# Kernel optimization log

Hardware: AMD Instinct MI355X
Metric: run time of the kernel (lower is better)

## Reference

```python
import jax, jax.numpy as jnp
import numpy as np

N, D, A, NQ, G1, G2 = 2048, 512, 64, 8, 8, 8
A1 = 2 * A  # tier-1 MQA uses att_dim*2 internally


def setup_inputs() -> dict:
    key = jax.random.key(0)
    ks = iter(jax.random.split(key, 24))
    r = lambda *sh: (jax.random.normal(next(ks), sh, dtype=jnp.float32) * 0.02)
    return {
        "x": jax.random.normal(next(ks), (N, D), dtype=jnp.float32),
        # tier 1 (num_groups_first MQA blocks, inner dim A1)
        "Wq1": r(G1, NQ, D, A1), "bq1": r(G1, NQ, A1),
        "Wk1": r(G1, D, A1),     "bk1": r(G1, A1),
        "Wv1": r(G1, D, A1),     "bv1": r(G1, A1),
        "Wo1": r(G1, NQ * A1, D), "bo1": r(G1, D),
        # tier 2 (num_groups_second MQA blocks, inner dim A)
        "Wq2": r(G2, NQ, D, A), "bq2": r(G2, NQ, A),
        "Wk2": r(G2, D, A),     "bk2": r(G2, A),
        "Wv2": r(G2, D, A),     "bv2": r(G2, A),
        "Wo2": r(G2, NQ * A, D), "bo2": r(G2, D),
        # final projection: in = att_dim * num_groups_second == D
        "Wo": r(D, D), "bo": r(D),
    }


def _mqa_grouped(xg, Wq, bq, Wk, bk, Wv, bv, Wo, bo):
    """Batched MultiQueryAttention over a group axis g.
    xg: [g, n, d]; Wq: [g, q, d, a]. No softmax (per source)."""
    a = Wq.shape[-1]
    q = jnp.einsum('gnd,gqda->gqna', xg, Wq) + bq[:, :, None, :]
    k = jnp.einsum('gnd,gda->gna', xg, Wk) + bk[:, None, :]
    v = jnp.einsum('gnd,gda->gna', xg, Wv) + bv[:, None, :]
    scores = jnp.einsum('gqna,gma->gqnm', q, k) / jnp.sqrt(jnp.asarray(a, jnp.float32))
    ctx = jnp.einsum('gqnm,gma->gqna', scores, v)          # [g,q,n,a]
    g, nq, n, ad = ctx.shape
    ctx = ctx.transpose(0, 2, 1, 3).reshape(g, n, nq * ad)  # concat queries on feat dim
    return jnp.einsum('gnf,gfd->gnd', ctx, Wo) + bo[:, None, :]


def reference(x, Wq1, bq1, Wk1, bk1, Wv1, bv1, Wo1, bo1,
              Wq2, bq2, Wk2, bk2, Wv2, bv2, Wo2, bo2, Wo, bo):
    xg = jnp.broadcast_to(x[None], (G1, N, D))
    o1 = _mqa_grouped(xg, Wq1, bq1, Wk1, bk1, Wv1, bv1, Wo1, bo1)   # [G1,N,D]
    o2 = _mqa_grouped(o1[:G2], Wq2, bq2, Wk2, bk2, Wv2, bv2, Wo2, bo2)  # [G2,N,D]
    o2_flat = o2.reshape(G2 * N, D)  # torch.cat along token dim (dim=0)
    return o2_flat @ Wo + bo          # [G2*N, D]
```

## Files before the change

kernel.cpp:

```cpp
#include <hip/hip_runtime.h>


typedef __bf16 bf16x8 __attribute__((ext_vector_type(8)));
typedef float  f32x4  __attribute__((ext_vector_type(4)));

struct PD { const float* s; void* d; int R, C, Bc, mode, blocks; };
struct PArgs { PD p[20]; int n; };

struct MA {
    const float *x,*bq1,*bo1,*bq2,*bo2,*bo;
    float* out;
    __bf16 *xb,*Wk1t,*Wv1t,*Wq1b,*Wo1t,*Wk2t,*Wv2t,*Wq2b,*Wo2b,*Wot;
    __bf16 *Ktb,*Vtb,*T1b,*M1t,*o1b,*K2tb,*V2tb,*T2b,*Wo2pT,*M2pt;
    float *STf1,*STf2,*kvb1,*kvb2,*c1,*c2p,*bo2p;
    PArgs pa;
    int prepTot;
};

template<int BM, int BN, int KK>
__device__ __forceinline__ void ss_gemm(void* smv,
    const __bf16* __restrict__ A, const float* __restrict__ Bf,
    __bf16* __restrict__ C, long aG, long bG, long cG, int cD, int cQ, int vb)
{
    constexpr int MT = BM / 32, NT = BN / 32, KS = KK / 32;
    constexpr int ACH = (KK * 2) / 16;
    constexpr int ABYTES = BM * KK * 2;
    constexpr int AITER = ABYTES / 16 / 256;
    constexpr int ROWB = KK * 2;
    constexpr int F4PT = (BN * KK) / 4 / 256;
    constexpr int TPR  = (KK / 4) / F4PT;

    char* smc = (char*)smv;
    int g = vb >> 6, rb = vb & 63;
    A  += g * aG + (long)rb * BM * KK;
    Bf += g * bG;
    C  += g * cG;

    int tid = threadIdx.x, wave = tid >> 6, lane = tid & 63;
    int mrow = lane & 15, quad = lane >> 4;

    #pragma unroll
    for (int i = 0; i < AITER; ++i) {
        int c = tid + i * 256;
        int row = c / ACH, cp = c % ACH;
        int cg = cp ^ (row & 7);
        __builtin_amdgcn_global_load_lds(
            (const __attribute__((address_space(1))) void*)(A + (long)row * KK + cg * 8),
            (__attribute__((address_space(3))) void*)(smc + c * 16),
            16, 0, 0);
    }
    {
        int brow = tid / TPR, bseg = tid % TPR;
        const float4* bsrc = (const float4*)(Bf + (long)brow * KK + bseg * (KK / TPR));
        int cbase = (bseg * (KK / TPR)) >> 3;
        int bx7 = brow & 7;
        char* bls = smc + ABYTES + (long)brow * ROWB;
        #pragma unroll
        for (int j = 0; j < F4PT / 2; ++j) {
            float4 f0 = bsrc[2 * j], f1 = bsrc[2 * j + 1];
            bf16x8 v = {(__bf16)f0.x, (__bf16)f0.y, (__bf16)f0.z, (__bf16)f0.w,
                        (__bf16)f1.x, (__bf16)f1.y, (__bf16)f1.z, (__bf16)f1.w};
            *(bf16x8*)(bls + (((cbase + j) ^ bx7) << 4)) = v;
        }
    }
    __syncthreads();

    int wm = (wave >> 1) * (BM / 2), wn = (wave & 1) * (BN / 2);
    f32x4 acc[MT][NT];
    #pragma unroll
    for (int i = 0; i < MT; ++i)
        #pragma unroll
        for (int j = 0; j < NT; ++j)
            acc[i][j] = f32x4{0.f, 0.f, 0.f, 0.f};

    #pragma unroll
    for (int ks = 0; ks < KS; ++ks) {
        bf16x8 af[MT], bv[NT];
        #pragma unroll
        for (int mt = 0; mt < MT; ++mt) {
            int r = wm + mt * 16 + mrow;
            af[mt] = *(const bf16x8*)(smc + (long)r * ROWB
                        + (((ks * 4 + quad) ^ (r & 7)) << 4));
        }
        #pragma unroll
        for (int nt = 0; nt < NT; ++nt) {
            int r = wn + nt * 16 + mrow;
            bv[nt] = *(const bf16x8*)(smc + ABYTES + (long)r * ROWB
                        + (((ks * 4 + quad) ^ (r & 7)) << 4));
        }
        #pragma unroll
        for (int mt = 0; mt < MT; ++mt)
            #pragma unroll
            for (int nt = 0; nt < NT; ++nt)
                acc[mt][nt] = __builtin_amdgcn_mfma_f32_16x16x32_bf16(
                    af[mt], bv[nt], acc[mt][nt], 0, 0, 0);
    }

    #pragma unroll
    for (int mt = 0; mt < MT; ++mt) {
        #pragma unroll
        for (int r4 = 0; r4 < 4; ++r4) {
            int rl = wm + mt * 16 + quad * 4 + r4;
            int ra = rb * BM + rl;
            int q = ra >> 9, d = ra & 511;
            #pragma unroll
            for (int nt = 0; nt < NT; ++nt) {
                int col = wn + nt * 16 + mrow;
                C[(long)d * cD + q * cQ + col] = (__bf16)acc[mt][nt][r4];
            }
        }
    }
}

template<int BM, int BN, bool BF32, int MODE>
__device__ __forceinline__ void gemm_block(void* smv,
    const __bf16* __restrict__ A, const void* __restrict__ Bv,
    const float* __restrict__ bias, void* __restrict__ Cv,
    int K, int lda, int ldb, int ldc, int divq, int ksplit,
    long aOut, long aIn, long bOut, long bIn, long cOut, long cIn,
    long biasOut, long biasIn, int hasBias, float alpha,
    int bx, int by, int bz)
{
    constexpr int MT = BM / 32, NT = BN / 32;
    constexpr int HALF = (BM + BN) * 64;
    constexpr int AL = BM / 64;
    constexpr int BL = BF32 ? 0 : BN / 64;

    char* smc = (char*)smv;

    int b  = bz / ksplit, ks = bz - b * ksplit;
    int go = b / divq,  gi = b - go * divq;
    A += go * aOut + gi * aIn;
    const __bf16* Bb = (const __bf16*)Bv + (BF32 ? 0 : (go * bOut + gi * bIn));
    const float*  Bf = (const float*)Bv + (BF32 ? (go * bOut + gi * bIn) : 0);
    long cBase = go * cOut + gi * cIn;
    if (hasBias) bias += go * biasOut + gi * biasIn;

    int kChunk = K / ksplit;
    int k0 = ks * kChunk;
    int nT = kChunk / 32;

    int bm = by * BM, bn = bx * BN;
    int tid = threadIdx.x, wave = tid >> 6, lane = tid & 63;
    int wm = (wave >> 1) * (BM / 2), wn = (wave & 1) * (BN / 2);
    int mrow = lane & 15, quad = lane >> 4;

    f32x4 acc[MT][NT];
    #pragma unroll
    for (int i = 0; i < MT; ++i)
        #pragma unroll
        for (int j = 0; j < NT; ++j)
            acc[i][j] = f32x4{0.f, 0.f, 0.f, 0.f};

    float4 bf0, bf1;
    int brow = tid >> 2, bcb = (tid & 3) * 8;

    auto loadBf32 = [&](int kk) {
        const float* src = Bf + (long)(bn + brow) * ldb + kk + bcb;
        bf0 = *(const float4*)(src);
        bf1 = *(const float4*)(src + 4);
    };
    auto writeBf32 = [&](int buf) {
        bf16x8 v = {(__bf16)bf0.x, (__bf16)bf0.y, (__bf16)bf0.z, (__bf16)bf0.w,
                    (__bf16)bf1.x, (__bf16)bf1.y, (__bf16)bf1.z, (__bf16)bf1.w};
        *(bf16x8*)(smc + buf * HALF + BM * 64 + brow * 64 + bcb * 2) = v;
    };
    auto issueAB = [&](int buf, int kk) {
        char* base = smc + buf * HALF;
        #pragma unroll
        for (int t = 0; t < AL; ++t) {
            int c = tid + t * 256;
            int row = c >> 2, kq = c & 3;
            __builtin_amdgcn_global_load_lds(
                (const __attribute__((address_space(1))) void*)
                    (A + (long)(bm + row) * lda + kk + kq * 8),
                (__attribute__((address_space(3))) void*)(base + row * 64 + kq * 16),
                16, 0, 0);
        }
        if constexpr (!BF32) {
            #pragma unroll
            for (int t = 0; t < BL; ++t) {
                int c = tid + t * 256;
                int row = c >> 2, kq = c & 3;
                __builtin_amdgcn_global_load_lds(
                    (const __attribute__((address_space(1))) void*)
                        (Bb + (long)(bn + row) * ldb + kk + kq * 8),
                    (__attribute__((address_space(3))) void*)
                        (base + BM * 64 + row * 64 + kq * 16),
                    16, 0, 0);
            }
        }
    };

    if constexpr (BF32) loadBf32(k0);
    issueAB(0, k0);
    if constexpr (BF32) writeBf32(0);
    __syncthreads();

    int cur = 0;
    for (int t = 0; t < nT; ++t) {
        int kk = k0 + (t + 1) * 32;
        if (t + 1 < nT) {
            if constexpr (BF32) loadBf32(kk);
            issueAB(cur ^ 1, kk);
        }

        char* base = smc + cur * HALF;
        bf16x8 af[MT], bfv[NT];
        #pragma unroll
        for (int mt = 0; mt < MT; ++mt)
            af[mt] = *(const bf16x8*)(base + (wm + mt * 16 + mrow) * 64 + quad * 16);
        #pragma unroll
        for (int nt = 0; nt < NT; ++nt)
            bfv[nt] = *(const bf16x8*)(base + BM * 64 + (wn + nt * 16 + mrow) * 64 + quad * 16);
        #pragma unroll
        for (int mt = 0; mt < MT; ++mt)
            #pragma unroll
            for (int nt = 0; nt < NT; ++nt) {
                if constexpr (MODE == 2)
                    acc[mt][nt] = __builtin_amdgcn_mfma_f32_16x16x32_bf16(
                        bfv[nt], af[mt], acc[mt][nt], 0, 0, 0);
                else
                    acc[mt][nt] = __builtin_amdgcn_mfma_f32_16x16x32_bf16(
                        af[mt], bfv[nt], acc[mt][nt], 0, 0, 0);
            }

        if constexpr (BF32) {
            if (t + 1 < nT) writeBf32(cur ^ 1);
        }

        __syncthreads();
        cur ^= 1;
    }

    if constexpr (MODE == 2) {
        #pragma unroll
        for (int nt = 0; nt < NT; ++nt) {
            #pragma unroll
            for (int r = 0; r < 4; ++r) {
                int ci = bn + wn + nt * 16 + quad * 4 + r;
                #pragma unroll
                for (int mt = 0; mt < MT; ++mt) {
                    int mi = bm + wm + mt * 16 + mrow;
                    float v = acc[mt][nt][r] * alpha;
                    if (hasBias) v += bias[ci];
                    ((__bf16*)Cv)[cBase + (long)ci * ldc + mi] = (__bf16)v;
                }
            }
        }
    } else {
        #pragma unroll
        for (int mt = 0; mt < MT; ++mt) {
            #pragma unroll
            for (int r = 0; r < 4; ++r) {
                int row = bm + wm + mt * 16 + quad * 4 + r;
                #pragma unroll
                for (int nt = 0; nt < NT; ++nt) {
                    int col = bn + wn + nt * 16 + mrow;
                    float v = acc[mt][nt][r] * alpha;
                    if (hasBias) v += bias[col];
                    if constexpr (MODE == 0)
                        ((float*)Cv)[cBase + (long)row * ldc + col] = v;
                    else if constexpr (MODE == 1)
                        ((__bf16*)Cv)[cBase + (long)row * ldc + col] = (__bf16)v;
                    else
                        atomicAdd(&((float*)Cv)[cBase + (long)row * ldc + col], v);
                }
            }
        }
    }
}

__device__ __forceinline__ void prep_block(const PArgs& a, int bid, void* smv)
{
    int i = 0;
    while (i < a.n && bid >= a.p[i].blocks) { bid -= a.p[i].blocks; ++i; }
    if (i >= a.n) return;
    PD d = a.p[i];
    int t = threadIdx.x;
    if (d.mode == 0) {
        float (*tile)[33] = (float(*)[33])smv;
        int tC = d.C >> 5, tR = d.R >> 5;
        int batch = bid / (tC * tR), rem = bid - batch * (tC * tR);
        int tyo = rem / tC, txo = rem - tyo * tC;
        const float* src = d.s + (long)batch * d.R * d.C;
        __bf16* dst = (__bf16*)d.d + (long)batch * d.R * d.C;
        int tx = t & 31, ty = t >> 5;
        int r0 = tyo * 32, c0 = txo * 32;
        #pragma unroll
        for (int u = 0; u < 4; ++u)
            tile[ty + 8 * u][tx] = src[(long)(r0 + ty + 8 * u) * d.C + c0 + tx];
        __syncthreads();
        #pragma unroll
        for (int u = 0; u < 4; ++u)
            dst[(long)(c0 + ty + 8 * u) * d.R + r0 + tx] = (__bf16)tile[tx][ty + 8 * u];
    } else if (d.mode == 1) {
        long idx = ((long)bid * 256 + t) * 4;
        long total = (long)d.Bc * d.R * d.C;
        if (idx < total) {
            float4 f = *(const float4*)(d.s + idx);
            __bf16* o = (__bf16*)d.d + idx;
            o[0] = (__bf16)f.x; o[1] = (__bf16)f.y;
            o[2] = (__bf16)f.z; o[3] = (__bf16)f.w;
        }
    } else {
        long idx = (long)bid * 256 + t;
        long total = (long)d.Bc * d.R * d.C;
        if (idx < total) {
            float* o = (float*)d.d;
            if (d.mode == 2) o[idx] = d.s[idx];
            else             o[idx] = 0.f;
        }
    }
}

__device__ __forceinline__ void small_block(void* smv,
    const float* __restrict__ STf, const float* __restrict__ bq,
    const __bf16* __restrict__ WoT, const float* __restrict__ boA,
    float* __restrict__ cOut, int ad, int F, long wG, int bid)
{
    int tid = threadIdx.x;
    float* rL  = (float*)smv;
    float* red = (float*)((char*)smv + 4096);
    int g = bid >> 5, slice = bid & 31;
    int nq = F / ad;
    const float* Sg = STf + (long)g * ad * ad;
    for (int f = tid; f < F; f += 256) {
        int q = f / ad, aa = f - q * ad;
        const float* bv = bq + (long)(g * nq + q) * ad;
        const float* Sa = Sg + (long)aa * ad;
        float s = 0.f;
        for (int c = 0; c < ad; c += 4) {
            float4 b4 = *(const float4*)(bv + c);
            float4 s4 = *(const float4*)(Sa + c);
            s += b4.x * s4.x + b4.y * s4.y + b4.z * s4.z + b4.w * s4.w;
        }
        rL[f] = s;
    }
    __syncthreads();
    int dl = tid & 15, fs = tid >> 4;
    int d = slice * 16 + dl;
    int fchunk = F >> 4;
    const __bf16* wrow = WoT + (long)g * wG + (long)d * F;
    float s = 0.f;
    for (int f0 = fs * fchunk; f0 < (fs + 1) * fchunk; f0 += 8) {
        bf16x8 w = *(const bf16x8*)(wrow + f0);
        s += rL[f0]     * (float)w[0] + rL[f0 + 1] * (float)w[1]
           + rL[f0 + 2] * (float)w[2] + rL[f0 + 3] * (float)w[3]
           + rL[f0 + 4] * (float)w[4] + rL[f0 + 5] * (float)w[5]
           + rL[f0 + 6] * (float)w[6] + rL[f0 + 7] * (float)w[7];
    }
    red[tid] = s;
    __syncthreads();
    if (fs == 0) {
        float tsum = s;
        #pragma unroll
        for (int u = 1; u < 16; ++u) tsum += red[u * 16 + dl];
        cOut[(long)g * 512 + d] = boA[(long)g * 512 + d] + tsum;
    }
}

__device__ __forceinline__ void vecmat_block(void* smv,
    const float* __restrict__ v, const __bf16* __restrict__ WT,
    const float* __restrict__ bias, float* __restrict__ outp, int g, int slice)
{
    float* red2 = (float*)smv;
    int tid = threadIdx.x;
    int dl = tid & 15, fs = tid >> 4;
    int d = slice * 16 + dl;
    const float* vg = v + (long)g * 512;
    const __bf16* wrow = WT + (long)d * 512;
    float s = 0.f;
    for (int f0 = fs * 32; f0 < (fs + 1) * 32; f0 += 8) {
        bf16x8 w = *(const bf16x8*)(wrow + f0);
        s += vg[f0]     * (float)w[0] + vg[f0 + 1] * (float)w[1]
           + vg[f0 + 2] * (float)w[2] + vg[f0 + 3] * (float)w[3]
           + vg[f0 + 4] * (float)w[4] + vg[f0 + 5] * (float)w[5]
           + vg[f0 + 6] * (float)w[6] + vg[f0 + 7] * (float)w[7];
    }
    red2[tid] = s;
    __syncthreads();
    if (fs == 0) {
        float tsum = s;
        #pragma unroll
        for (int u = 1; u < 16; ++u) tsum += red2[u * 16 + dl];
        outp[(long)g * 512 + d] = bias[d] + tsum;
    }
}

template<int S>
__device__ __forceinline__ void run_stage(const MA& a, int vb, void* sm)
{
    const float isa1 = 0.08838834764831845f;
    if constexpr (S == 0) {
        prep_block(a.pa, vb, sm);
    } else if constexpr (S == 1) {
        if (vb < 1024)
            gemm_block<64,64,false,2>(sm, a.xb, a.Wk1t, a.kvb1, a.Ktb,
                512, 512, 512, 2048, 1, 1,
                0L, 0L, 65536L, 0L, 262144L, 0L, 128L, 0L, 1, 1.0f,
                vb & 1, (vb >> 1) & 31, vb >> 6);
        else if (vb < 1536) {
            int v = vb - 1024;
            gemm_block<64,64,false,2>(sm, a.Wo2b, a.Wot, nullptr, a.Wo2pT,
                512, 512, 512, 512, 1, 1,
                262144L, 0L, 0L, 0L, 262144L, 0L, 0L, 0L, 0, 1.0f,
                v & 7, (v >> 3) & 7, v >> 6);
        } else {
            int v = vb - 1536;
            vecmat_block(sm, a.bo2, a.Wot, a.bo, a.bo2p, v & 7, v >> 3);
        }
    } else if constexpr (S == 2) {
        gemm_block<64,64,false,3>(sm, a.Vtb, a.Ktb, nullptr, a.STf1,
            2048, 2048, 2048, 128, 1, 8,
            262144L, 0L, 262144L, 0L, 16384L, 0L, 0L, 0L, 0, isa1,
            vb & 1, (vb >> 1) & 1, vb >> 2);
    } else if constexpr (S == 3) {
        if (vb < 512)
            ss_gemm<64,128,128>(sm, a.Wq1b, a.STf1, a.T1b,
                                524288L, 16384L, 524288L, 1024, 128, vb);
        else
            small_block(sm, a.STf1, a.bq1, a.Wo1t, a.bo1, a.c1,
                        128, 1024, 524288L, vb - 512);
    } else if constexpr (S == 4) {
        gemm_block<64,64,false,2>(sm, a.T1b, a.Wo1t, nullptr, a.M1t,
            1024, 1024, 1024, 512, 1, 1,
            524288L, 0L, 524288L, 0L, 262144L, 0L, 0L, 0L, 0, 1.0f,
            vb & 7, (vb >> 3) & 7, vb >> 6);
    } else if constexpr (S == 5) {
        gemm_block<128,128,false,1>(sm, a.xb, a.M1t, a.c1, a.o1b,
            512, 512, 512, 512, 1, 1,
            0L, 0L, 262144L, 0L, 1048576L, 0L, 512L, 0L, 1, 1.0f,
            vb & 3, (vb >> 2) & 15, vb >> 6);
    } else if constexpr (S == 6) {
        gemm_block<64,64,false,2>(sm, a.o1b, a.Wk2t, a.kvb2, a.K2tb,
            512, 512, 512, 2048, 8, 1,
            0L, 1048576L, 262144L, 32768L, 1048576L, 131072L, 512L, 64L,
            1, 1.0f, 0, vb & 31, vb >> 5);
    } else if constexpr (S == 7) {
        gemm_block<64,64,false,3>(sm, a.V2tb, a.K2tb, nullptr, a.STf2,
            2048, 2048, 2048, 64, 1, 16,
            131072L, 0L, 131072L, 0L, 4096L, 0L, 0L, 0L, 0, 0.125f,
            0, 0, vb);
    } else if constexpr (S == 8) {
        if (vb < 512)
            ss_gemm<64,64,64>(sm, a.Wq2b, a.STf2, a.T2b,
                              262144L, 4096L, 262144L, 512, 64, vb);
        else
            small_block(sm, a.STf2, a.bq2, a.Wo2pT, a.bo2p, a.c2p,
                        64, 512, 262144L, vb - 512);
    } else if constexpr (S == 9) {
        gemm_block<64,64,false,2>(sm, a.T2b, a.Wo2pT, nullptr, a.M2pt,
            512, 512, 512, 512, 1, 1,
            262144L, 0L, 262144L, 0L, 262144L, 0L, 0L, 0L, 0, 1.0f,
            vb & 7, (vb >> 3) & 7, vb >> 6);
    } else {
        gemm_block<128,128,false,0>(sm, a.o1b, a.M2pt, a.c2p, a.out,
            512, 512, 512, 512, 1, 1,
            1048576L, 0L, 262144L, 0L, 1048576L, 0L, 512L, 0L, 1, 1.0f,
            vb & 3, (vb >> 2) & 15, vb >> 6);
    }
}

#define STAGE_KERNEL(NAME, S, SMEM)                                          \
__global__ __launch_bounds__(256, 4) void NAME(MA a)                         \
{                                                                            \
    __shared__ __align__(16) unsigned char smem[SMEM];                       \
    run_stage<S>(a, blockIdx.x, smem);                                       \
}

STAGE_KERNEL(ksg0_prep,    0, 16384)
STAGE_KERNEL(ksg1_kv1wo2p, 1, 16384)
STAGE_KERNEL(ksg2_s1t,     2, 16384)
STAGE_KERNEL(ksg3_t1c1,    3, 49152)
STAGE_KERNEL(ksg4_m1t,     4, 16384)
STAGE_KERNEL(ksg5_o1,      5, 32768)
STAGE_KERNEL(ksg6_kv2,     6, 16384)
STAGE_KERNEL(ksg7_s2t,     7, 16384)
STAGE_KERNEL(ksg8_t2c2p,   8, 16384)
STAGE_KERNEL(ksg9_m2pt,    9, 16384)
STAGE_KERNEL(ksg10_out,   10, 32768)

extern "C" void kernel_launch(void* const* d_in, const int* in_sizes, int n_in,
                              void* d_out, int out_size, void* d_ws, size_t ws_size,
                              hipStream_t stream)
{
    MA ma;
    ma.x   = (const float*)d_in[0];
    const float* Wq1 = (const float*)d_in[1];  ma.bq1 = (const float*)d_in[2];
    const float* Wk1 = (const float*)d_in[3];  const float* bk1 = (const float*)d_in[4];
    const float* Wv1 = (const float*)d_in[5];  const float* bv1 = (const float*)d_in[6];
    const float* Wo1 = (const float*)d_in[7];  ma.bo1 = (const float*)d_in[8];
    const float* Wq2 = (const float*)d_in[9];  ma.bq2 = (const float*)d_in[10];
    const float* Wk2 = (const float*)d_in[11]; const float* bk2 = (const float*)d_in[12];
    const float* Wv2 = (const float*)d_in[13]; const float* bv2 = (const float*)d_in[14];
    const float* Wo2 = (const float*)d_in[15]; ma.bo2 = (const float*)d_in[16];
    const float* Wo  = (const float*)d_in[17]; ma.bo  = (const float*)d_in[18];
    ma.out = (float*)d_out;
    (void)in_sizes; (void)n_in; (void)out_size; (void)ws_size;

    __bf16* wb = (__bf16*)d_ws;
    long o = 0;
    ma.xb    = wb + o; o += 1048576;
    ma.Wk1t  = wb + o; o += 524288;
    ma.Wv1t  = wb + o; o += 524288;
    ma.Wq1b  = wb + o; o += 4194304;
    ma.Wo1t  = wb + o; o += 4194304;
    ma.Wk2t  = wb + o; o += 262144;
    ma.Wv2t  = wb + o; o += 262144;
    ma.Wq2b  = wb + o; o += 2097152;
    ma.Wo2b  = wb + o; o += 2097152;
    ma.Wot   = wb + o; o += 262144;
    ma.Ktb   = wb + o; o += 2097152;
    ma.Vtb   = wb + o; o += 2097152;
    ma.T1b   = wb + o; o += 4194304;
    ma.M1t   = wb + o; o += 2097152;
    ma.o1b   = wb + o; o += 8388608;
    ma.K2tb  = ma.Ktb;
    ma.V2tb  = ma.Ktb + 1048576;
    ma.T2b   = wb + o; o += 2097152;
    ma.Wo2pT = wb + o; o += 2097152;
    ma.M2pt  = wb + o; o += 2097152;
    float* wf = (float*)(wb + o);
    long p = 0;
    ma.STf1 = wf + p; p += 131072;
    ma.STf2 = wf + p; p += 32768;
    ma.kvb1 = wf + p; p += 2048;
    ma.kvb2 = wf + p; p += 1024;
    ma.c1   = wf + p; p += 4096;
    ma.c2p  = wf + p; p += 4096;
    ma.bo2p = wf + p; p += 4096;

    int nd = 0, totB = 0;
    auto add = [&](const float* s, void* d, int R, int C, int Bc, int mode) {
        int blocks;
        long total = (long)Bc * R * C;
        if (mode == 0) blocks = Bc * (R >> 5) * (C >> 5);
        else if (mode == 1) blocks = (int)(total / 1024);
        else blocks = (int)((total + 255) / 256);
        ma.pa.p[nd] = PD{s, d, R, C, Bc, mode, blocks};
        ++nd; totB += blocks;
    };
    add(ma.x, ma.xb,   2048, 512, 1, 1);
    add(Wq1,  ma.Wq1b, 512, 128, 64, 1);
    add(Wq2,  ma.Wq2b, 512, 64, 64, 1);
    add(Wo2,  ma.Wo2b, 512, 512, 8, 1);
    add(Wk1,  ma.Wk1t, 512, 128, 8, 0);
    add(Wv1,  ma.Wv1t, 512, 128, 8, 0);
    add(Wo1,  ma.Wo1t, 1024, 512, 8, 0);
    add(Wk2,  ma.Wk2t, 512, 64, 8, 0);
    add(Wv2,  ma.Wv2t, 512, 64, 8, 0);
    add(Wo,   ma.Wot,  512, 512, 1, 0);
    add(bk1,  ma.kvb1,        1, 1024, 1, 2);
    add(bv1,  ma.kvb1 + 1024, 1, 1024, 1, 2);
    add(bk2,  ma.kvb2,        1, 512, 1, 2);
    add(bv2,  ma.kvb2 + 512,  1, 512, 1, 2);
    add(nullptr, ma.STf1, 1, 131072, 1, 4);
    add(nullptr, ma.STf2, 1, 32768, 1, 4);
    ma.pa.n = nd;
    ma.prepTot = totB;

    ksg0_prep   <<<dim3(ma.prepTot), dim3(256), 0, stream>>>(ma);
    ksg1_kv1wo2p<<<dim3(1792), dim3(256), 0, stream>>>(ma);
    ksg2_s1t    <<<dim3(256),  dim3(256), 0, stream>>>(ma);
    ksg3_t1c1   <<<dim3(768),  dim3(256), 0, stream>>>(ma);
    ksg4_m1t    <<<dim3(512),  dim3(256), 0, stream>>>(ma);
    ksg5_o1     <<<dim3(512),  dim3(256), 0, stream>>>(ma);
    ksg6_kv2    <<<dim3(512),  dim3(256), 0, stream>>>(ma);
    ksg7_s2t    <<<dim3(128),  dim3(256), 0, stream>>>(ma);
    ksg8_t2c2p  <<<dim3(768),  dim3(256), 0, stream>>>(ma);
    ksg9_m2pt   <<<dim3(512),  dim3(256), 0, stream>>>(ma);
    ksg10_out   <<<dim3(512),  dim3(256), 0, stream>>>(ma);
}
```

Before: 267.8 us.

## Use 64-wide K tiles with XOR-swizzled LDS layout in shared GEMM

The shared GEMM block now stages 64-element K slices per iteration instead of 32, so it runs half as many barrier-separated steps. Each slice is a 128-byte LDS row whose 16-byte chunks are XOR-swizzled by row, which is meant to avoid LDS bank conflicts on the fragment reads. The unused fp32-B conversion path is removed. LDS per block doubles and the two 128x128 stages lower their launch-bounds occupancy hint to 2, which may cut the number of resident waves.

```diff
diff --git a/kernel.cpp b/kernel.cpp
--- a/kernel.cpp
+++ b/kernel.cpp
@@ -112,9 +112,9 @@
     }
 }
 
-template<int BM, int BN, bool BF32, int MODE>
+template<int BM, int BN, int MODE>
 __device__ __forceinline__ void gemm_block(void* smv,
-    const __bf16* __restrict__ A, const void* __restrict__ Bv,
+    const __bf16* __restrict__ A, const __bf16* __restrict__ B,
     const float* __restrict__ bias, void* __restrict__ Cv,
     int K, int lda, int ldb, int ldc, int divq, int ksplit,
     long aOut, long aIn, long bOut, long bIn, long cOut, long cIn,
@@ -122,23 +122,23 @@
     int bx, int by, int bz)
 {
     constexpr int MT = BM / 32, NT = BN / 32;
-    constexpr int HALF = (BM + BN) * 64;
-    constexpr int AL = BM / 64;
-    constexpr int BL = BF32 ? 0 : BN / 64;
+    constexpr int ROWB = 128;
+    constexpr int HALF = (BM + BN) * ROWB;
+    constexpr int AOPS = BM * 8 / 256;
+    constexpr int BOPS = BN * 8 / 256;
 
     char* smc = (char*)smv;
 
     int b  = bz / ksplit, ks = bz - b * ksplit;
     int go = b / divq,  gi = b - go * divq;
     A += go * aOut + gi * aIn;
-    const __bf16* Bb = (const __bf16*)Bv + (BF32 ? 0 : (go * bOut + gi * bIn));
-    const float*  Bf = (const float*)Bv + (BF32 ? (go * bOut + gi * bIn) : 0);
+    B += go * bOut + gi * bIn;
     long cBase = go * cOut + gi * cIn;
     if (hasBias) bias += go * biasOut + gi * biasIn;
 
     int kChunk = K / ksplit;
     int k0 = ks * kChunk;
-    int nT = kChunk / 32;
+    int nT = kChunk / 64;
 
     int bm = by * BM, bn = bx * BN;
     int tid = threadIdx.x, wave = tid >> 6, lane = tid & 63;
@@ -152,81 +152,67 @@
         for (int j = 0; j < NT; ++j)
             acc[i][j] = f32x4{0.f, 0.f, 0.f, 0.f};
 
-    float4 bf0, bf1;
-    int brow = tid >> 2, bcb = (tid & 3) * 8;
-
-    auto loadBf32 = [&](int kk) {
-        const float* src = Bf + (long)(bn + brow) * ldb + kk + bcb;
-        bf0 = *(const float4*)(src);
-        bf1 = *(const float4*)(src + 4);
-    };
-    auto writeBf32 = [&](int buf) {
-        bf16x8 v = {(__bf16)bf0.x, (__bf16)bf0.y, (__bf16)bf0.z, (__bf16)bf0.w,
-                    (__bf16)bf1.x, (__bf16)bf1.y, (__bf16)bf1.z, (__bf16)bf1.w};
-        *(bf16x8*)(smc + buf * HALF + BM * 64 + brow * 64 + bcb * 2) = v;
-    };
     auto issueAB = [&](int buf, int kk) {
         char* base = smc + buf * HALF;
         #pragma unroll
-        for (int t = 0; t < AL; ++t) {
+        for (int t = 0; t < AOPS; ++t) {
             int c = tid + t * 256;
-            int row = c >> 2, kq = c & 3;
+            int row = c >> 3, cp = c & 7;
+            int cg = cp ^ (row & 7);
             __builtin_amdgcn_global_load_lds(
                 (const __attribute__((address_space(1))) void*)
-                    (A + (long)(bm + row) * lda + kk + kq * 8),
-                (__attribute__((address_space(3))) void*)(base + row * 64 + kq * 16),
+                    (A + (long)(bm + row) * lda + kk + cg * 8),
+                (__attribute__((address_space(3))) void*)(base + c * 16),
                 16, 0, 0);
         }
-        if constexpr (!BF32) {
-            #pragma unroll
-            for (int t = 0; t < BL; ++t) {
-                int c = tid + t * 256;
-                int row = c >> 2, kq = c & 3;
-                __builtin_amdgcn_global_load_lds(
-                    (const __attribute__((address_space(1))) void*)
-                        (Bb + (long)(bn + row) * ldb + kk + kq * 8),
-                    (__attribute__((address_space(3))) void*)
-                        (base + BM * 64 + row * 64 + kq * 16),
-                    16, 0, 0);
-            }
+        char* bbase = base + BM * ROWB;
+        #pragma unroll
+        for (int t = 0; t < BOPS; ++t) {
+            int c = tid + t * 256;
+            int row = c >> 3, cp = c & 7;
+            int cg = cp ^ (row & 7);
+            __builtin_amdgcn_global_load_lds(
+                (const __attribute__((address_space(1))) void*)
+                    (B + (long)(bn + row) * ldb + kk + cg * 8),
+                (__attribute__((address_space(3))) void*)(bbase + c * 16),
+                16, 0, 0);
         }
     };
 
-    if constexpr (BF32) loadBf32(k0);
     issueAB(0, k0);
-    if constexpr (BF32) writeBf32(0);
     __syncthreads();
 
     int cur = 0;
     for (int t = 0; t < nT; ++t) {
-        int kk = k0 + (t + 1) * 32;
-        if (t + 1 < nT) {
-            if constexpr (BF32) loadBf32(kk);
-            issueAB(cur ^ 1, kk);
-        }
+        if (t + 1 < nT) issueAB(cur ^ 1, k0 + (t + 1) * 64);
 
         char* base = smc + cur * HALF;
-        bf16x8 af[MT], bfv[NT];
-        #pragma unroll
-        for (int mt = 0; mt < MT; ++mt)
-            af[mt] = *(const bf16x8*)(base + (wm + mt * 16 + mrow) * 64 + quad * 16);
-        #pragma unroll
-        for (int nt = 0; nt < NT; ++nt)
-            bfv[nt] = *(const bf16x8*)(base + BM * 64 + (wn + nt * 16 + mrow) * 64 + quad * 16);
-        #pragma unroll
-        for (int mt = 0; mt < MT; ++mt)
+        #pragma unroll
+        for (int k2 = 0; k2 < 2; ++k2) {
+            bf16x8 af[MT], bfv[NT];
+            #pragma unroll
+            for (int mt = 0; mt < MT; ++mt) {
+                int r = wm + mt * 16 + mrow;
+                af[mt] = *(const bf16x8*)(base + r * ROWB
+                            + (((k2 * 4 + quad) ^ (r & 7)) << 4));
+            }
             #pragma unroll
             for (int nt = 0; nt < NT; ++nt) {
-                if constexpr (MODE == 2)
-                    acc[mt][nt] = __builtin_amdgcn_mfma_f32_16x16x32_bf16(
-                        bfv[nt], af[mt], acc[mt][nt], 0, 0, 0);
-                else
-                    acc[mt][nt] = __builtin_amdgcn_mfma_f32_16x16x32_bf16(
-                        af[mt], bfv[nt], acc[mt][nt], 0, 0, 0);
+                int r = wn + nt * 16 + mrow;
+                bfv[nt] = *(const bf16x8*)(base + BM * ROWB + r * ROWB
+                            + (((k2 * 4 + quad) ^ (r & 7)) << 4));
             }
-
-        if constexpr (BF32) {
-            if (t + 1 < nT) writeBf32(cur ^ 1);
+            #pragma unroll
+            for (int mt = 0; mt < MT; ++mt)
+                #pragma unroll
+                for (int nt = 0; nt < NT; ++nt) {
+                    if constexpr (MODE == 2)
+                        acc[mt][nt] = __builtin_amdgcn_mfma_f32_16x16x32_bf16(
+                            bfv[nt], af[mt], acc[mt][nt], 0, 0, 0);
+                    else
+                        acc[mt][nt] = __builtin_amdgcn_mfma_f32_16x16x32_bf16(
+                            af[mt], bfv[nt], acc[mt][nt], 0, 0, 0);
+                }
         }
 
         __syncthreads();
@@ -396,13 +382,13 @@
         prep_block(a.pa, vb, sm);
     } else if constexpr (S == 1) {
         if (vb < 1024)
-            gemm_block<64,64,false,2>(sm, a.xb, a.Wk1t, a.kvb1, a.Ktb,
+            gemm_block<64,64,2>(sm, a.xb, a.Wk1t, a.kvb1, a.Ktb,
                 512, 512, 512, 2048, 1, 1,
                 0L, 0L, 65536L, 0L, 262144L, 0L, 128L, 0L, 1, 1.0f,
                 vb & 1, (vb >> 1) & 31, vb >> 6);
         else if (vb < 1536) {
             int v = vb - 1024;
-            gemm_block<64,64,false,2>(sm, a.Wo2b, a.Wot, nullptr, a.Wo2pT,
+            gemm_block<64,64,2>(sm, a.Wo2b, a.Wot, nullptr, a.Wo2pT,
                 512, 512, 512, 512, 1, 1,
                 262144L, 0L, 0L, 0L, 262144L, 0L, 0L, 0L, 0, 1.0f,
                 v & 7, (v >> 3) & 7, v >> 6);
@@ -411,7 +397,7 @@
             vecmat_block(sm, a.bo2, a.Wot, a.bo, a.bo2p, v & 7, v >> 3);
         }
     } else if constexpr (S == 2) {
-        gemm_block<64,64,false,3>(sm, a.Vtb, a.Ktb, nullptr, a.STf1,
+        gemm_block<64,64,3>(sm, a.Vtb, a.Ktb, nullptr, a.STf1,
             2048, 2048, 2048, 128, 1, 8,
             262144L, 0L, 262144L, 0L, 16384L, 0L, 0L, 0L, 0, isa1,
             vb & 1, (vb >> 1) & 1, vb >> 2);
@@ -423,22 +409,22 @@
             small_block(sm, a.STf1, a.bq1, a.Wo1t, a.bo1, a.c1,
                         128, 1024, 524288L, vb - 512);
     } else if constexpr (S == 4) {
-        gemm_block<64,64,false,2>(sm, a.T1b, a.Wo1t, nullptr, a.M1t,
+        gemm_block<64,64,2>(sm, a.T1b, a.Wo1t, nullptr, a.M1t,
             1024, 1024, 1024, 512, 1, 1,
             524288L, 0L, 524288L, 0L, 262144L, 0L, 0L, 0L, 0, 1.0f,
             vb & 7, (vb >> 3) & 7, vb >> 6);
     } else if constexpr (S == 5) {
-        gemm_block<128,128,false,1>(sm, a.xb, a.M1t, a.c1, a.o1b,
+        gemm_block<128,128,1>(sm, a.xb, a.M1t, a.c1, a.o1b,
             512, 512, 512, 512, 1, 1,
             0L, 0L, 262144L, 0L, 1048576L, 0L, 512L, 0L, 1, 1.0f,
             vb & 3, (vb >> 2) & 15, vb >> 6);
     } else if constexpr (S == 6) {
-        gemm_block<64,64,false,2>(sm, a.o1b, a.Wk2t, a.kvb2, a.K2tb,
+        gemm_block<64,64,2>(sm, a.o1b, a.Wk2t, a.kvb2, a.K2tb,
             512, 512, 512, 2048, 8, 1,
             0L, 1048576L, 262144L, 32768L, 1048576L, 131072L, 512L, 64L,
             1, 1.0f, 0, vb & 31, vb >> 5);
     } else if constexpr (S == 7) {
-        gemm_block<64,64,false,3>(sm, a.V2tb, a.K2tb, nullptr, a.STf2,
+        gemm_block<64,64,3>(sm, a.V2tb, a.K2tb, nullptr, a.STf2,
             2048, 2048, 2048, 64, 1, 16,
             131072L, 0L, 131072L, 0L, 4096L, 0L, 0L, 0L, 0, 0.125f,
             0, 0, vb);
@@ -450,36 +436,36 @@
             small_block(sm, a.STf2, a.bq2, a.Wo2pT, a.bo2p, a.c2p,
                         64, 512, 262144L, vb - 512);
     } else if constexpr (S == 9) {
-        gemm_block<64,64,false,2>(sm, a.T2b, a.Wo2pT, nullptr, a.M2pt,
+        gemm_block<64,64,2>(sm, a.T2b, a.Wo2pT, nullptr, a.M2pt,
             512, 512, 512, 512, 1, 1,
             262144L, 0L, 262144L, 0L, 262144L, 0L, 0L, 0L, 0, 1.0f,
             vb & 7, (vb >> 3) & 7, vb >> 6);
     } else {
-        gemm_block<128,128,false,0>(sm, a.o1b, a.M2pt, a.c2p, a.out,
+        gemm_block<128,128,0>(sm, a.o1b, a.M2pt, a.c2p, a.out,
             512, 512, 512, 512, 1, 1,
             1048576L, 0L, 262144L, 0L, 1048576L, 0L, 512L, 0L, 1, 1.0f,
             vb & 3, (vb >> 2) & 15, vb >> 6);
     }
 }
 
-#define STAGE_KERNEL(NAME, S, SMEM)                                          \
-__global__ __launch_bounds__(256, 4) void NAME(MA a)                         \
+#define STAGE_KERNEL(NAME, S, SMEM, MINW)                                    \
+__global__ __launch_bounds__(256, MINW) void NAME(MA a)                      \
 {                                                                            \
     __shared__ __align__(16) unsigned char smem[SMEM];                       \
     run_stage<S>(a, blockIdx.x, smem);                                       \
 }
 
-STAGE_KERNEL(ksg0_prep,    0, 16384)
-STAGE_KERNEL(ksg1_kv1wo2p, 1, 16384)
-STAGE_KERNEL(ksg2_s1t,     2, 16384)
-STAGE_KERNEL(ksg3_t1c1,    3, 49152)
-STAGE_KERNEL(ksg4_m1t,     4, 16384)
-STAGE_KERNEL(ksg5_o1,      5, 32768)
-STAGE_KERNEL(ksg6_kv2,     6, 16384)
-STAGE_KERNEL(ksg7_s2t,     7, 16384)
-STAGE_KERNEL(ksg8_t2c2p,   8, 16384)
-STAGE_KERNEL(ksg9_m2pt,    9, 16384)
-STAGE_KERNEL(ksg10_out,   10, 32768)
+STAGE_KERNEL(ksg0_prep,    0, 16384, 4)
+STAGE_KERNEL(ksg1_kv1wo2p, 1, 32768, 4)
+STAGE_KERNEL(ksg2_s1t,     2, 32768, 4)
+STAGE_KERNEL(ksg3_t1c1,    3, 49152, 4)
+STAGE_KERNEL(ksg4_m1t,     4, 32768, 4)
+STAGE_KERNEL(ksg5_o1,      5, 65536, 2)
+STAGE_KERNEL(ksg6_kv2,     6, 32768, 4)
+STAGE_KERNEL(ksg7_s2t,     7, 32768, 4)
+STAGE_KERNEL(ksg8_t2c2p,   8, 16384, 4)
+STAGE_KERNEL(ksg9_m2pt,    9, 32768, 4)
+STAGE_KERNEL(ksg10_out,   10, 65536, 2)
 
 extern "C" void kernel_launch(void* const* d_in, const int* in_sizes, int n_in,
                               void* d_out, int out_size, void* d_ws, size_t ws_size,
```

After: 257.0 us (median of 2 runs). 4.0% less time.
